# Optimization experiments

Hardware: AMD Instinct MI355X
Metric: run time of the kernel (lower is better)

The kernel has to match this reference:

```python
import jax, jax.numpy as jnp
import numpy as np

WS = 9       # window_size
GAMMA = 2.0
REAL = False


def box_avg(x, ws):
    """Depthwise uniform box filter with circular padding, weight = 1/ws^2."""
    p = ws // 2
    xp = jnp.pad(x, ((0, 0), (0, 0), (p, p), (p, p)), mode='wrap')  # circular pad
    c = x.shape[1]
    k = jnp.full((c, 1, ws, ws), 1.0 / (ws * ws), dtype=x.dtype)
    return jax.lax.conv_general_dilated(
        xp, k, window_strides=(1, 1), padding='VALID',
        dimension_numbers=('NCHW', 'OIHW', 'NCHW'), feature_group_count=c)


def local_variance(x, ws):
    # E[x^2] - (E[x])^2 per channel over the circular box window
    return box_avg(x * x, ws) - jnp.square(box_avg(x, ws))


def setup_inputs() -> dict:
    key = jax.random.key(0)
    x = jax.random.normal(key, (16, 3, 512, 512), dtype=jnp.float32)
    return {"x": x}


def reference(x):
    # alpha_map: mean over channels of per-channel local variance of x
    alpha_map = local_variance(x, WS).sum(1, keepdims=True) / 3
    # beta_map: local variance of the channel-mean image
    beta_map = local_variance(x.sum(1, keepdims=True) / 3, WS)
    # weight map from variance of x - x with channels reversed ([2,1,0])
    weight = local_variance(x - x[:, ::-1], WS).sum(1, keepdims=True) / 3
    _, _, w, h = weight.shape
    w_sum = weight.sum()
    weight = jnp.exp(-GAMMA * w * h * weight / w_sum)
    w_sum = weight.sum()
    scale = 9.0 / 4.0 if REAL else 3.0 / 2.0
    return scale * (weight * (alpha_map - beta_map)).sum() / w_sum
```

## Files before the change

kernel.cpp:

```cpp
#include <hip/hip_runtime.h>
#include <math.h>

#define N_ 16
#define C_ 3
#define H_ 512
#define W_ 512
#define HW_ (H_ * W_)
#define PLANE_ (N_ * HW_)
#define BAND 8
#define GAMMA_ 2.0f

__device__ __forceinline__ float wave_reduce(float v) {
#pragma unroll
    for (int off = 32; off > 0; off >>= 1)
        v += __shfl_down(v, off, 64);
    return v;
}

template <int MODE>
__global__ __launch_bounds__(256) void pass1(const float* __restrict__ x,
                                             float* __restrict__ wr_plane,
                                             float* __restrict__ diff_plane,
                                             float* __restrict__ scalars) {
    __shared__ float rowbuf[6][W_];
    __shared__ float red[8];

    const int tid = threadIdx.x;
    const int c0 = tid * 2;
    const int y0 = blockIdx.x * BAND;
    const int b = blockIdx.y;
    const float* xb = x + (size_t)b * (C_ * HW_);

    float coef = 0.0f;
    if (MODE == 2) coef = GAMMA_ * (float)HW_ / scalars[0];

    float vs[6][2];
#pragma unroll
    for (int f = 0; f < 6; ++f) vs[f][0] = vs[f][1] = 0.0f;

    auto row_update = [&](int r, float sgn) {
        int rr = r & (H_ - 1);
        const float* p = xb + rr * W_ + c0;
        float2 a0 = *(const float2*)(p);
        float2 a1 = *(const float2*)(p + HW_);
        float2 a2 = *(const float2*)(p + 2 * HW_);
#pragma unroll
        for (int i = 0; i < 2; ++i) {
            float x0 = i ? a0.y : a0.x;
            float x1 = i ? a1.y : a1.x;
            float x2 = i ? a2.y : a2.x;
            float yv = (x0 + x1 + x2) * (1.0f / 3.0f);
            float d = x0 - x2;
            vs[0][i] = fmaf(sgn, x0, vs[0][i]);
            vs[1][i] = fmaf(sgn, x1, vs[1][i]);
            vs[2][i] = fmaf(sgn, x2, vs[2][i]);
            vs[3][i] = fmaf(sgn, x0 * x0 + x1 * x1 + x2 * x2, vs[3][i]);
            vs[4][i] = fmaf(sgn, yv * yv, vs[4][i]);
            vs[5][i] = fmaf(sgn, d * d, vs[5][i]);
        }
    };

#pragma unroll
    for (int k = 0; k < 9; ++k) row_update(y0 - 4 + k, 1.0f);

    float accwr = 0.0f, accw = 0.0f, accwd = 0.0f;
    const float inv81 = 1.0f / 81.0f;

    for (int y = y0; y < y0 + BAND; ++y) {
#pragma unroll
        for (int f = 0; f < 6; ++f)
            *(float2*)&rowbuf[f][c0] = make_float2(vs[f][0], vs[f][1]);
        __syncthreads();

        float hs[6][2];
#pragma unroll
        for (int f = 0; f < 6; ++f) {
            float2 v[5];
#pragma unroll
            for (int j = 0; j < 5; ++j)
                v[j] = *(const float2*)&rowbuf[f][(c0 + 2 * j - 4) & (W_ - 1)];
            float s0 = ((v[0].x + v[0].y) + (v[1].x + v[1].y)) +
                       ((v[2].x + v[2].y) + (v[3].x + v[3].y)) + v[4].x;
            float s1 = s0 - v[0].x + v[4].y;
            hs[f][0] = s0;
            hs[f][1] = s1;
        }

        float wrv[2], dfv[2];
#pragma unroll
        for (int i = 0; i < 2; ++i) {
            float B0 = hs[0][i] * inv81, B1 = hs[1][i] * inv81, B2 = hs[2][i] * inv81;
            float alpha = (hs[3][i] * inv81 - (B0 * B0 + B1 * B1 + B2 * B2)) * (1.0f / 3.0f);
            float my = (B0 + B1 + B2) * (1.0f / 3.0f);
            float beta = hs[4][i] * inv81 - my * my;
            float md = B0 - B2;
            float wr = (2.0f / 3.0f) * (hs[5][i] * inv81 - md * md);
            float df = alpha - beta;
            wrv[i] = wr;
            dfv[i] = df;
            if (MODE <= 1) {
                accwr += wr;
            } else {
                float w = __expf(-coef * wr);
                accw += w;
                accwd += w * df;
            }
        }
        if (MODE == 0) {
            int gidx = b * HW_ + y * W_ + c0;
            *(float2*)&wr_plane[gidx] = make_float2(wrv[0], wrv[1]);
            *(float2*)&diff_plane[gidx] = make_float2(dfv[0], dfv[1]);
        }
        __syncthreads();

        if (y + 1 < y0 + BAND) {
            row_update(y + 5, 1.0f);
            row_update(y - 4, -1.0f);
        }
    }

    if (MODE <= 1) {
        float s = wave_reduce(accwr);
        if ((tid & 63) == 0) red[tid >> 6] = s;
        __syncthreads();
        if (tid == 0) atomicAdd(&scalars[0], (red[0] + red[1]) + (red[2] + red[3]));
    } else {
        float s0 = wave_reduce(accw);
        float s1 = wave_reduce(accwd);
        if ((tid & 63) == 0) {
            red[tid >> 6] = s0;
            red[4 + (tid >> 6)] = s1;
        }
        __syncthreads();
        if (tid == 0) {
            atomicAdd(&scalars[1], (red[0] + red[1]) + (red[2] + red[3]));
            atomicAdd(&scalars[2], (red[4] + red[5]) + (red[6] + red[7]));
        }
    }
}

__global__ __launch_bounds__(256) void weight_kernel(const float* __restrict__ wr_plane,
                                                     const float* __restrict__ diff_plane,
                                                     float* __restrict__ scalars) {
    __shared__ float red[8];
    const float coef = GAMMA_ * (float)HW_ / scalars[0];
    const float4* wr4 = (const float4*)wr_plane;
    const float4* df4 = (const float4*)diff_plane;
    const int n4 = PLANE_ / 4;
    float sw = 0.0f, swd = 0.0f;
    int stride = gridDim.x * blockDim.x;
    for (int i = blockIdx.x * blockDim.x + threadIdx.x; i < n4; i += stride) {
        float4 a = wr4[i];
        float4 d = df4[i];
        float w0 = __expf(-coef * a.x);
        float w1 = __expf(-coef * a.y);
        float w2 = __expf(-coef * a.z);
        float w3 = __expf(-coef * a.w);
        sw += (w0 + w1) + (w2 + w3);
        swd += (w0 * d.x + w1 * d.y) + (w2 * d.z + w3 * d.w);
    }
    sw = wave_reduce(sw);
    swd = wave_reduce(swd);
    int tid = threadIdx.x;
    if ((tid & 63) == 0) {
        red[tid >> 6] = sw;
        red[4 + (tid >> 6)] = swd;
    }
    __syncthreads();
    if (tid == 0) {
        atomicAdd(&scalars[1], (red[0] + red[1]) + (red[2] + red[3]));
        atomicAdd(&scalars[2], (red[4] + red[5]) + (red[6] + red[7]));
    }
}

__global__ void final_kernel(const float* __restrict__ scalars, float* __restrict__ out) {
    out[0] = 1.5f * scalars[2] / scalars[1];
}

extern "C" void kernel_launch(void* const* d_in, const int* in_sizes, int n_in,
                              void* d_out, int out_size, void* d_ws, size_t ws_size,
                              hipStream_t stream) {
    const float* x = (const float*)d_in[0];
    float* out = (float*)d_out;
    float* scalars = (float*)d_ws;

    hipMemsetAsync(d_ws, 0, 16, stream);

    dim3 grid(H_ / BAND, N_);
    const size_t need = 256 + 2 * (size_t)PLANE_ * sizeof(float);

    if (ws_size >= need) {
        float* wr_plane = (float*)((char*)d_ws + 256);
        float* diff_plane = wr_plane + PLANE_;
        pass1<0><<<grid, 256, 0, stream>>>(x, wr_plane, diff_plane, scalars);
        weight_kernel<<<1024, 256, 0, stream>>>(wr_plane, diff_plane, scalars);
    } else {
        pass1<1><<<grid, 256, 0, stream>>>(x, nullptr, nullptr, scalars);
        pass1<2><<<grid, 256, 0, stream>>>(x, nullptr, nullptr, scalars);
    }
    final_kernel<<<1, 1, 0, stream>>>(scalars, out);
}
```

Baseline: 136.5 us.

## Replace materialized planes with lightweight sum pass and recomputing second pass

Removes the intermediate wr/diff plane writes and the separate weight kernel. A light first pass reads only channels 0 and 2 to compute the global weight sum, and a second pass recomputes all box statistics from x to accumulate the exp-weighted sums. This trades 32 MB of plane writes and rereads for recomputing the stencil and rereading x, which may hit in cache.

```diff
diff --git a/kernel.cpp b/kernel.cpp
--- a/kernel.cpp
+++ b/kernel.cpp
@@ -2,11 +2,9 @@
 #include <math.h>
 
 #define N_ 16
-#define C_ 3
 #define H_ 512
 #define W_ 512
 #define HW_ (H_ * W_)
-#define PLANE_ (N_ * HW_)
 #define BAND 8
 #define GAMMA_ 2.0f
 
@@ -17,22 +15,91 @@
     return v;
 }
 
-template <int MODE>
-__global__ __launch_bounds__(256) void pass1(const float* __restrict__ x,
-                                             float* __restrict__ wr_plane,
-                                             float* __restrict__ diff_plane,
+__global__ __launch_bounds__(256) void passA(const float* __restrict__ x,
                                              float* __restrict__ scalars) {
-    __shared__ float rowbuf[6][W_];
-    __shared__ float red[8];
+    __shared__ float rowbuf[3][W_];
+    __shared__ float red[4];
 
     const int tid = threadIdx.x;
     const int c0 = tid * 2;
     const int y0 = blockIdx.x * BAND;
     const int b = blockIdx.y;
-    const float* xb = x + (size_t)b * (C_ * HW_);
-
-    float coef = 0.0f;
-    if (MODE == 2) coef = GAMMA_ * (float)HW_ / scalars[0];
+    const float* xb = x + (size_t)b * (3 * HW_);
+    const float inv81 = 1.0f / 81.0f;
+
+    float va[3][2];
+#pragma unroll
+    for (int f = 0; f < 3; ++f) va[f][0] = va[f][1] = 0.0f;
+
+    auto rowlite = [&](int r, float sgn) {
+        int rr = r & (H_ - 1);
+        const float* p = xb + rr * W_ + c0;
+        float2 a0 = *(const float2*)(p);
+        float2 a2 = *(const float2*)(p + 2 * HW_);
+#pragma unroll
+        for (int i = 0; i < 2; ++i) {
+            float x0 = i ? a0.y : a0.x;
+            float x2 = i ? a2.y : a2.x;
+            float d = x0 - x2;
+            va[0][i] = fmaf(sgn, x0, va[0][i]);
+            va[1][i] = fmaf(sgn, x2, va[1][i]);
+            va[2][i] = fmaf(sgn, d * d, va[2][i]);
+        }
+    };
+
+#pragma unroll
+    for (int k = 0; k < 9; ++k) rowlite(y0 - 4 + k, 1.0f);
+
+    float accwr = 0.0f;
+    for (int y = y0; y < y0 + BAND; ++y) {
+#pragma unroll
+        for (int f = 0; f < 3; ++f)
+            *(float2*)&rowbuf[f][c0] = make_float2(va[f][0], va[f][1]);
+        __syncthreads();
+
+        float hs[3][2];
+#pragma unroll
+        for (int f = 0; f < 3; ++f) {
+            float2 v[5];
+#pragma unroll
+            for (int j = 0; j < 5; ++j)
+                v[j] = *(const float2*)&rowbuf[f][(c0 + 2 * j - 4) & (W_ - 1)];
+            float s0 = ((v[0].x + v[0].y) + (v[1].x + v[1].y)) +
+                       ((v[2].x + v[2].y) + (v[3].x + v[3].y)) + v[4].x;
+            hs[f][0] = s0;
+            hs[f][1] = s0 - v[0].x + v[4].y;
+        }
+#pragma unroll
+        for (int i = 0; i < 2; ++i) {
+            float md = (hs[0][i] - hs[1][i]) * inv81;
+            accwr += (2.0f / 3.0f) * (hs[2][i] * inv81 - md * md);
+        }
+        __syncthreads();
+
+        if (y + 1 < y0 + BAND) {
+            rowlite(y + 5, 1.0f);
+            rowlite(y - 4, -1.0f);
+        }
+    }
+
+    float s = wave_reduce(accwr);
+    if ((tid & 63) == 0) red[tid >> 6] = s;
+    __syncthreads();
+    if (tid == 0) atomicAdd(&scalars[0], (red[0] + red[1]) + (red[2] + red[3]));
+}
+
+__global__ __launch_bounds__(256) void passB(const float* __restrict__ x,
+                                             float* __restrict__ scalars) {
+    __shared__ float rowbuf[6][W_];
+    __shared__ float red[8];
+
+    const int tid = threadIdx.x;
+    const int c0 = tid * 2;
+    const int y0 = blockIdx.x * BAND;
+    const int b = blockIdx.y;
+    const float* xb = x + (size_t)b * (3 * HW_);
+    const float inv81 = 1.0f / 81.0f;
+    const float coef = GAMMA_ * (float)HW_ / scalars[0];
 
     float vs[6][2];
 #pragma unroll
@@ -63,8 +130,7 @@
 #pragma unroll
     for (int k = 0; k < 9; ++k) row_update(y0 - 4 + k, 1.0f);
 
-    float accwr = 0.0f, accw = 0.0f, accwd = 0.0f;
-    const float inv81 = 1.0f / 81.0f;
+    float accw = 0.0f, accwd = 0.0f;
 
     for (int y = y0; y < y0 + BAND; ++y) {
 #pragma unroll
@@ -81,12 +147,10 @@
                 v[j] = *(const float2*)&rowbuf[f][(c0 + 2 * j - 4) & (W_ - 1)];
             float s0 = ((v[0].x + v[0].y) + (v[1].x + v[1].y)) +
                        ((v[2].x + v[2].y) + (v[3].x + v[3].y)) + v[4].x;
-            float s1 = s0 - v[0].x + v[4].y;
             hs[f][0] = s0;
-            hs[f][1] = s1;
-        }
-
-        float wrv[2], dfv[2];
+            hs[f][1] = s0 - v[0].x + v[4].y;
+        }
+
 #pragma unroll
         for (int i = 0; i < 2; ++i) {
             float B0 = hs[0][i] * inv81, B1 = hs[1][i] * inv81, B2 = hs[2][i] * inv81;
@@ -96,20 +160,9 @@
             float md = B0 - B2;
             float wr = (2.0f / 3.0f) * (hs[5][i] * inv81 - md * md);
             float df = alpha - beta;
-            wrv[i] = wr;
-            dfv[i] = df;
-            if (MODE <= 1) {
-                accwr += wr;
-            } else {
-                float w = __expf(-coef * wr);
-                accw += w;
-                accwd += w * df;
-            }
-        }
-        if (MODE == 0) {
-            int gidx = b * HW_ + y * W_ + c0;
-            *(float2*)&wr_plane[gidx] = make_float2(wrv[0], wrv[1]);
-            *(float2*)&diff_plane[gidx] = make_float2(dfv[0], dfv[1]);
+            float w = __expf(-coef * wr);
+            accw += w;
+            accwd += w * df;
         }
         __syncthreads();
 
@@ -119,52 +172,11 @@
         }
     }
 
-    if (MODE <= 1) {
-        float s = wave_reduce(accwr);
-        if ((tid & 63) == 0) red[tid >> 6] = s;
-        __syncthreads();
-        if (tid == 0) atomicAdd(&scalars[0], (red[0] + red[1]) + (red[2] + red[3]));
-    } else {
-        float s0 = wave_reduce(accw);
-        float s1 = wave_reduce(accwd);
-        if ((tid & 63) == 0) {
-            red[tid >> 6] = s0;
-            red[4 + (tid >> 6)] = s1;
-        }
-        __syncthreads();
-        if (tid == 0) {
-            atomicAdd(&scalars[1], (red[0] + red[1]) + (red[2] + red[3]));
-            atomicAdd(&scalars[2], (red[4] + red[5]) + (red[6] + red[7]));
-        }
-    }
-}
-
-__global__ __launch_bounds__(256) void weight_kernel(const float* __restrict__ wr_plane,
-                                                     const float* __restrict__ diff_plane,
-                                                     float* __restrict__ scalars) {
-    __shared__ float red[8];
-    const float coef = GAMMA_ * (float)HW_ / scalars[0];
-    const float4* wr4 = (const float4*)wr_plane;
-    const float4* df4 = (const float4*)diff_plane;
-    const int n4 = PLANE_ / 4;
-    float sw = 0.0f, swd = 0.0f;
-    int stride = gridDim.x * blockDim.x;
-    for (int i = blockIdx.x * blockDim.x + threadIdx.x; i < n4; i += stride) {
-        float4 a = wr4[i];
-        float4 d = df4[i];
-        float w0 = __expf(-coef * a.x);
-        float w1 = __expf(-coef * a.y);
-        float w2 = __expf(-coef * a.z);
-        float w3 = __expf(-coef * a.w);
-        sw += (w0 + w1) + (w2 + w3);
-        swd += (w0 * d.x + w1 * d.y) + (w2 * d.z + w3 * d.w);
-    }
-    sw = wave_reduce(sw);
-    swd = wave_reduce(swd);
-    int tid = threadIdx.x;
+    float s0 = wave_reduce(accw);
+    float s1 = wave_reduce(accwd);
     if ((tid & 63) == 0) {
-        red[tid >> 6] = sw;
-        red[4 + (tid >> 6)] = swd;
+        red[tid >> 6] = s0;
+        red[4 + (tid >> 6)] = s1;
     }
     __syncthreads();
     if (tid == 0) {
@@ -187,16 +199,7 @@
     hipMemsetAsync(d_ws, 0, 16, stream);
 
     dim3 grid(H_ / BAND, N_);
-    const size_t need = 256 + 2 * (size_t)PLANE_ * sizeof(float);
-
-    if (ws_size >= need) {
-        float* wr_plane = (float*)((char*)d_ws + 256);
-        float* diff_plane = wr_plane + PLANE_;
-        pass1<0><<<grid, 256, 0, stream>>>(x, wr_plane, diff_plane, scalars);
-        weight_kernel<<<1024, 256, 0, stream>>>(wr_plane, diff_plane, scalars);
-    } else {
-        pass1<1><<<grid, 256, 0, stream>>>(x, nullptr, nullptr, scalars);
-        pass1<2><<<grid, 256, 0, stream>>>(x, nullptr, nullptr, scalars);
-    }
+    passA<<<grid, 256, 0, stream>>>(x, scalars);
+    passB<<<grid, 256, 0, stream>>>(x, scalars);
     final_kernel<<<1, 1, 0, stream>>>(scalars, out);
 }
```

New measurement: 139.2 us. Within noise of the previous version (+2.0%).
